# Kernel tuning notes

Measured on AMD Instinct MI355X. Metric: run time of the kernel, lower is better.

## Reference

```python
import jax, jax.numpy as jnp
import numpy as np

N = 4096
CIN = 128
COUT = 128
J = 2
SLOPE = 0.2        # LeakyReLU negative slope (GAT-style)
NEG = -9.0e15      # mask fill value from the source
ATT = J * COUT     # att_slice


def _leaky(v):
    return jnp.where(v >= 0, v, SLOPE * v)


def setup_inputs() -> dict:
    key = jax.random.key(0)
    ks = jax.random.split(key, 12)
    x = jax.random.normal(ks[0], (N, CIN), dtype=jnp.float32)

    def sparse_op(k):
        kv, km = jax.random.split(k)
        vals = jax.random.normal(kv, (N, N), dtype=jnp.float32)
        mask = jax.random.uniform(km, (N, N)) < 0.05
        return jnp.where(mask, vals, 0.0)

    Lu = sparse_op(ks[1])
    Ld = sparse_op(ks[2])
    P = jax.random.normal(ks[3], (N, N), dtype=jnp.float32) * 0.01  # harmonic projector

    s = 1.0 / np.sqrt(CIN)
    Wi_w = jax.random.uniform(ks[4], (J, CIN, COUT), minval=-s, maxval=s)
    Wi_b = jax.random.uniform(ks[5], (J, COUT), minval=-s, maxval=s)
    Ws_w = jax.random.uniform(ks[6], (J, CIN, COUT), minval=-s, maxval=s)
    Ws_b = jax.random.uniform(ks[7], (J, COUT), minval=-s, maxval=s)
    Wh_w = jax.random.uniform(ks[8], (CIN, COUT), minval=-s, maxval=s)
    Wh_b = jax.random.uniform(ks[9], (COUT,), minval=-s, maxval=s)
    att_irr = jax.random.normal(ks[10], (2 * ATT, 1), dtype=jnp.float32) * 0.1
    att_sol = jax.random.normal(ks[11], (2 * ATT, 1), dtype=jnp.float32) * 0.1
    return {"x": x, "Lu": Lu, "Ld": Ld, "P": P,
            "Wi_w": Wi_w, "Wi_b": Wi_b, "Ws_w": Ws_w, "Ws_b": Ws_b,
            "Wh_w": Wh_w, "Wh_b": Wh_b, "att_irr": att_irr, "att_sol": att_sol}


def reference(x, Lu, Ld, P, Wi_w, Wi_b, Ws_w, Ws_b, Wh_w, Wh_b, att_irr, att_sol):
    n = x.shape[0]
    # concat_j W_irr[j](x) -> [N, J*COUT] (j-major matches torch.cat along dim=1)
    x_irr = (jnp.einsum('nc,jco->njo', x, Wi_w) + Wi_b[None]).reshape(n, ATT)
    x_sol = (jnp.einsum('nc,jco->njo', x, Ws_w) + Ws_b[None]).reshape(n, ATT)

    # GAT-style scores: E[i,j] = leaky(s1[i] + s2[j])
    E_irr = _leaky(x_irr @ att_irr[:ATT] + (x_irr @ att_irr[ATT:]).T)
    E_sol = _leaky(x_sol @ att_sol[:ATT] + (x_sol @ att_sol[ATT:]).T)
    E_irr = jnp.where(Ld != 0, E_irr, NEG)
    E_sol = jnp.where(Lu != 0, E_sol, NEG)
    alpha_irr = jax.nn.softmax(E_irr, axis=1)  # dropout: eval mode -> identity
    alpha_sol = jax.nn.softmax(E_sol, axis=1)

    z = (alpha_irr @ x) @ Wi_w[0] + Wi_b[0] + (alpha_sol @ x) @ Ws_w[0] + Ws_b[0]
    for p in range(1, J):  # Laplacian-power aggregation
        alpha_irr = alpha_irr @ Ld
        alpha_sol = alpha_sol @ Lu
        z = z + (alpha_irr @ x) @ Wi_w[p] + Wi_b[p]
        z = z + (alpha_sol @ x) @ Ws_w[p] + Ws_b[p]
    z = z + (P @ x) @ Wh_w + Wh_b
    return z
```

## Files before the change

kernel.cpp:

```cpp
#include <hip/hip_runtime.h>

#define NN 4096
#define CAP 384
#define SLOPE 0.2f

#define V_OFF     0
#define C_OFF     512
#define BT_OFF    516
#define S_OFF     1024
#define HXI_OFF   32768
#define HXS_OFF   (HXI_OFF + NN*128)
#define UI_OFF    (HXS_OFF + NN*128)
#define US_OFF    (UI_OFF + NN*128)
#define XWH_OFF   (US_OFF + NN*128)
#define OI_OFF    (XWH_OFF + NN*128)
#define OS_OFF    (OI_OFF + NN*128)
#define ZP_OFF    (OS_OFF + NN*128)
#define WS_FLOATS (ZP_OFF + 8*NN*128)
#define IDX_BYTE_OFF ((size_t)WS_FLOATS * 4)
#define VAL_BYTE_OFF (IDX_BYTE_OFF + (size_t)2*NN*CAP*2)
#define CNT_BYTE_OFF (VAL_BYTE_OFF + (size_t)2*NN*CAP*4)

__global__ __launch_bounds__(128) void k_prep(
    const float* __restrict__ Wi_w, const float* __restrict__ Wi_b,
    const float* __restrict__ Ws_w, const float* __restrict__ Ws_b,
    const float* __restrict__ Wh_b, const float* __restrict__ att_irr,
    const float* __restrict__ att_sol, float* __restrict__ ws) {
  const int t = threadIdx.x;
  float v1i = 0.f, v2i = 0.f, v1s = 0.f, v2s = 0.f;
  for (int j = 0; j < 2; ++j) {
    for (int o = 0; o < 128; ++o) {
      const float wi = Wi_w[j*16384 + t*128 + o];
      const float wv = Ws_w[j*16384 + t*128 + o];
      v1i += wi * att_irr[j*128 + o];
      v2i += wi * att_irr[256 + j*128 + o];
      v1s += wv * att_sol[j*128 + o];
      v2s += wv * att_sol[256 + j*128 + o];
    }
  }
  ws[V_OFF + t]       = v1i;
  ws[V_OFF + 128 + t] = v2i;
  ws[V_OFF + 256 + t] = v1s;
  ws[V_OFF + 384 + t] = v2s;
  ws[BT_OFF + t] = Wi_b[t] + Wi_b[128 + t] + Ws_b[t] + Ws_b[128 + t] + Wh_b[t];
  if (t < 4) {
    const float* bb = (t < 2) ? Wi_b : Ws_b;
    const float* aa = ((t < 2) ? att_irr : att_sol) + ((t & 1) ? 256 : 0);
    float c = 0.f;
    for (int k = 0; k < 256; ++k) c += bb[k] * aa[k];
    ws[C_OFF + t] = c;
  }
}

__global__ __launch_bounds__(256) void k_scores(const float* __restrict__ x,
                                                float* __restrict__ ws) {
  const int wave = threadIdx.x >> 6, lane = threadIdx.x & 63;
  const int row = blockIdx.x * 4 + wave;
  const float* v = ws + V_OFF;
  const float x0 = x[row*128 + lane];
  const float x1 = x[row*128 + 64 + lane];
  float p0 = x0 * v[lane]       + x1 * v[64 + lane];
  float p1 = x0 * v[128 + lane] + x1 * v[192 + lane];
  float p2 = x0 * v[256 + lane] + x1 * v[320 + lane];
  float p3 = x0 * v[384 + lane] + x1 * v[448 + lane];
  #pragma unroll
  for (int off = 32; off; off >>= 1) {
    p0 += __shfl_down(p0, off);
    p1 += __shfl_down(p1, off);
    p2 += __shfl_down(p2, off);
    p3 += __shfl_down(p3, off);
  }
  if (lane == 0) {
    ws[S_OFF + row]          = p0 + ws[C_OFF + 0];
    ws[S_OFF + NN + row]     = p1 + ws[C_OFF + 1];
    ws[S_OFF + 2*NN + row]   = p2 + ws[C_OFF + 2];
    ws[S_OFF + 3*NN + row]   = p3 + ws[C_OFF + 3];
  }
}

__global__ __launch_bounds__(256) void k_zero(int* __restrict__ cnt) {
  cnt[blockIdx.x * 256 + threadIdx.x] = 0;
}

__global__ __launch_bounds__(256) void k_csr(
    const float* __restrict__ Ld, const float* __restrict__ Lu,
    int* __restrict__ cntbuf, unsigned short* __restrict__ idxb,
    float* __restrict__ valb) {
  const int w = threadIdx.x >> 6, lane = threadIdx.x & 63;
  const int W = blockIdx.x * 4 + w;
  const int br = W >> 14;
  const int row = (W >> 2) & (NN - 1);
  const int quarter = W & 3;
  const float4* __restrict__ L4 =
      (const float4*)((br ? Lu : Ld) + (size_t)row * NN + quarter * 1024);
  float4 lv[4];
  #pragma unroll
  for (int i = 0; i < 4; ++i) lv[i] = L4[i*64 + lane];

  unsigned long long m[16];
  int runs[16];
  int run = 0;
  #pragma unroll
  for (int i = 0; i < 4; ++i)
    #pragma unroll
    for (int c = 0; c < 4; ++c) {
      const int r = i*4 + c;
      m[r] = __ballot((&lv[i].x)[c] != 0.f);
      runs[r] = run;
      run += (int)__popcll(m[r]);
    }
  int base = 0;
  if (lane == 0 && run) base = atomicAdd(&cntbuf[br*NN + row], run);
  base = __shfl(base, 0);
  const size_t rb = (size_t)(br*NN + row) * CAP;
  const unsigned long long lmask = (1ull << lane) - 1ull;
  #pragma unroll
  for (int i = 0; i < 4; ++i)
    #pragma unroll
    for (int c = 0; c < 4; ++c) {
      const int r = i*4 + c;
      const float v = (&lv[i].x)[c];
      if (v != 0.f) {
        const int pos = base + runs[r] + (int)__popcll(m[r] & lmask);
        if (pos < CAP) {
          idxb[rb + pos] = (unsigned short)(quarter*1024 + (i*64 + lane)*4 + c);
          valb[rb + pos] = v;
        }
      }
    }
}

__global__ __launch_bounds__(256) void k_gather_hx(
    const float* __restrict__ Ld, const float* __restrict__ Lu,
    const float* __restrict__ x, float* __restrict__ ws,
    const unsigned short* __restrict__ idxb, const float* __restrict__ valb,
    const int* __restrict__ cntbuf) {
  const int w = threadIdx.x >> 6, lane = threadIdx.x & 63;
  const int W = blockIdx.x * 4 + w;
  const int br = W >> 12;
  const int row = W & (NN - 1);
  const float2* __restrict__ x2 = (const float2*)x;
  float2* __restrict__ Hx2 = (float2*)(ws + (br ? HXS_OFF : HXI_OFF));
  const int cnt = cntbuf[br*NN + row];
  float a0 = 0.f, a1 = 0.f;
  if (cnt <= CAP) {
    const size_t rb = (size_t)(br*NN + row) * CAP;
    int jv[6]; float vv[6];
    #pragma unroll
    for (int s = 0; s < 6; ++s) {
      const int p = s*64 + lane;
      const bool in = p < cnt;
      jv[s] = in ? (int)idxb[rb + p] : 0;
      vv[s] = in ? valb[rb + p] : 0.f;
    }
    #pragma unroll
    for (int s = 0; s < 6; ++s) {
      if (s*64 < cnt) {
        const int qn = min(64, cnt - s*64);
        const int jvs = jv[s]; const float vvs = vv[s];
        int q = 0;
        for (; q + 8 <= qn; q += 8) {
          const int j0=__shfl(jvs,q+0), j1=__shfl(jvs,q+1), j2=__shfl(jvs,q+2), j3=__shfl(jvs,q+3);
          const int j4=__shfl(jvs,q+4), j5=__shfl(jvs,q+5), j6=__shfl(jvs,q+6), j7=__shfl(jvs,q+7);
          const float v0=__shfl(vvs,q+0), v1=__shfl(vvs,q+1), v2=__shfl(vvs,q+2), v3=__shfl(vvs,q+3);
          const float v4=__shfl(vvs,q+4), v5=__shfl(vvs,q+5), v6=__shfl(vvs,q+6), v7=__shfl(vvs,q+7);
          const float2 g0=x2[j0*64+lane], g1=x2[j1*64+lane], g2=x2[j2*64+lane], g3=x2[j3*64+lane];
          const float2 g4=x2[j4*64+lane], g5=x2[j5*64+lane], g6=x2[j6*64+lane], g7=x2[j7*64+lane];
          a0+=v0*g0.x; a1+=v0*g0.y; a0+=v1*g1.x; a1+=v1*g1.y;
          a0+=v2*g2.x; a1+=v2*g2.y; a0+=v3*g3.x; a1+=v3*g3.y;
          a0+=v4*g4.x; a1+=v4*g4.y; a0+=v5*g5.x; a1+=v5*g5.y;
          a0+=v6*g6.x; a1+=v6*g6.y; a0+=v7*g7.x; a1+=v7*g7.y;
        }
        for (; q < qn; ++q) {
          const int j = __shfl(jvs, q); const float v = __shfl(vvs, q);
          const float2 g = x2[j*64+lane];
          a0 += v*g.x; a1 += v*g.y;
        }
      }
    }
  } else {
    const float* __restrict__ Lrow = (br ? Lu : Ld) + (size_t)row * NN;
    for (int j = 0; j < NN; ++j) {
      const float v = Lrow[j];
      if (v != 0.f) { const float2 g = x2[j*64+lane]; a0 += v*g.x; a1 += v*g.y; }
    }
  }
  float2 o; o.x = a0; o.y = a1;
  Hx2[row*64 + lane] = o;
}

__global__ __launch_bounds__(256) void k_ugemm(
    const float* __restrict__ x, const float* __restrict__ Wi_w,
    const float* __restrict__ Ws_w, const float* __restrict__ Wh_w,
    float* __restrict__ ws) {
  const int rb = blockIdx.x;
  const int sel = blockIdx.y;
  const float* A[2]; const float* W[2]; int npass; float* out;
  if (sel == 0)      { A[0]=x; W[0]=Wi_w; A[1]=ws+HXI_OFF; W[1]=Wi_w+16384; npass=2; out=ws+UI_OFF; }
  else if (sel == 1) { A[0]=x; W[0]=Ws_w; A[1]=ws+HXS_OFF; W[1]=Ws_w+16384; npass=2; out=ws+US_OFF; }
  else               { A[0]=x; W[0]=Wh_w; A[1]=nullptr;    W[1]=nullptr;    npass=1; out=ws+XWH_OFF; }

  __shared__ __align__(16) float At[32][33];
  __shared__ __align__(16) float Wt[32][132];
  const int t = threadIdx.x;
  const int rg = t >> 4, cg = t & 15;
  const int r0 = rb * 32;
  float acc[2][8];
  #pragma unroll
  for (int i = 0; i < 2; ++i)
    #pragma unroll
    for (int j = 0; j < 8; ++j) acc[i][j] = 0.f;

  for (int ps = 0; ps < npass; ++ps) {
    const float* __restrict__ Ap = A[ps];
    const float* __restrict__ Wp = W[ps];
    for (int k0 = 0; k0 < 128; k0 += 32) {
      __syncthreads();
      { const int row = t >> 3, kq = t & 7;
        const float4 av = *(const float4*)&Ap[(r0 + row)*128 + k0 + kq*4];
        At[row][kq*4+0] = av.x; At[row][kq*4+1] = av.y;
        At[row][kq*4+2] = av.z; At[row][kq*4+3] = av.w; }
      #pragma unroll
      for (int l = 0; l < 4; ++l) {
        const int idx = t + l*256;
        const int kr = idx >> 5, c4 = idx & 31;
        const float4 wv = *(const float4*)&Wp[(k0 + kr)*128 + c4*4];
        Wt[kr][c4*4+0] = wv.x; Wt[kr][c4*4+1] = wv.y;
        Wt[kr][c4*4+2] = wv.z; Wt[kr][c4*4+3] = wv.w;
      }
      __syncthreads();
      #pragma unroll
      for (int k = 0; k < 32; ++k) {
        const float a0 = At[rg*2 + 0][k];
        const float a1 = At[rg*2 + 1][k];
        const float4 b0 = *(const float4*)&Wt[k][cg*8];
        const float4 b1 = *(const float4*)&Wt[k][cg*8 + 4];
        acc[0][0] += a0*b0.x; acc[0][1] += a0*b0.y; acc[0][2] += a0*b0.z; acc[0][3] += a0*b0.w;
        acc[0][4] += a0*b1.x; acc[0][5] += a0*b1.y; acc[0][6] += a0*b1.z; acc[0][7] += a0*b1.w;
        acc[1][0] += a1*b0.x; acc[1][1] += a1*b0.y; acc[1][2] += a1*b0.z; acc[1][3] += a1*b0.w;
        acc[1][4] += a1*b1.x; acc[1][5] += a1*b1.y; acc[1][6] += a1*b1.z; acc[1][7] += a1*b1.w;
      }
    }
  }
  #pragma unroll
  for (int i = 0; i < 2; ++i) {
    const int r = r0 + rg*2 + i;
    #pragma unroll
    for (int j = 0; j < 8; ++j) out[r*128 + cg*8 + j] = acc[i][j];
  }
}

__global__ __launch_bounds__(256) void k_pgemm(const float* __restrict__ P,
                                               const float* __restrict__ ws,
                                               float* __restrict__ zpart) {
  const int rbl = blockIdx.x;
  const int kz  = blockIdx.y;
  const float* __restrict__ Xw = ws + XWH_OFF;

  __shared__ __align__(16) float At[32][68];
  __shared__ __align__(16) float Xt[32][132];
  const int t = threadIdx.x;
  const int rg = t >> 4, cg = t & 15;
  const int r0 = rbl * 64;
  const int kbase = kz * 512;
  float acc[4][8];
  #pragma unroll
  for (int i = 0; i < 4; ++i)
    #pragma unroll
    for (int j = 0; j < 8; ++j) acc[i][j] = 0.f;

  for (int k0 = kbase; k0 < kbase + 512; k0 += 32) {
    __syncthreads();
    #pragma unroll
    for (int l = 0; l < 2; ++l) {
      const int idx = t + l*256;
      const int row = idx >> 3, kq = idx & 7;
      const float4 pv = *(const float4*)&P[(size_t)(r0 + row)*NN + k0 + kq*4];
      At[kq*4+0][row] = pv.x; At[kq*4+1][row] = pv.y;
      At[kq*4+2][row] = pv.z; At[kq*4+3][row] = pv.w;
    }
    #pragma unroll
    for (int l = 0; l < 4; ++l) {
      const int idx = t + l*256;
      const int kr = idx >> 5, c4 = idx & 31;
      const float4 xv = *(const float4*)&Xw[(k0 + kr)*128 + c4*4];
      Xt[kr][c4*4+0] = xv.x; Xt[kr][c4*4+1] = xv.y;
      Xt[kr][c4*4+2] = xv.z; Xt[kr][c4*4+3] = xv.w;
    }
    __syncthreads();
    #pragma unroll
    for (int k = 0; k < 32; ++k) {
      const float4 a  = *(const float4*)&At[k][rg*4];
      const float4 b0 = *(const float4*)&Xt[k][cg*8];
      const float4 b1 = *(const float4*)&Xt[k][cg*8 + 4];
      acc[0][0] += a.x*b0.x; acc[0][1] += a.x*b0.y; acc[0][2] += a.x*b0.z; acc[0][3] += a.x*b0.w;
      acc[0][4] += a.x*b1.x; acc[0][5] += a.x*b1.y; acc[0][6] += a.x*b1.z; acc[0][7] += a.x*b1.w;
      acc[1][0] += a.y*b0.x; acc[1][1] += a.y*b0.y; acc[1][2] += a.y*b0.z; acc[1][3] += a.y*b0.w;
      acc[1][4] += a.y*b1.x; acc[1][5] += a.y*b1.y; acc[1][6] += a.y*b1.z; acc[1][7] += a.y*b1.w;
      acc[2][0] += a.z*b0.x; acc[2][1] += a.z*b0.y; acc[2][2] += a.z*b0.z; acc[2][3] += a.z*b0.w;
      acc[2][4] += a.z*b1.x; acc[2][5] += a.z*b1.y; acc[2][6] += a.z*b1.z; acc[2][7] += a.z*b1.w;
      acc[3][0] += a.w*b0.x; acc[3][1] += a.w*b0.y; acc[3][2] += a.w*b0.z; acc[3][3] += a.w*b0.w;
      acc[3][4] += a.w*b1.x; acc[3][5] += a.w*b1.y; acc[3][6] += a.w*b1.z; acc[3][7] += a.w*b1.w;
    }
  }
  float* __restrict__ zp = zpart + (size_t)kz * NN * 128;
  #pragma unroll
  for (int i = 0; i < 4; ++i) {
    const int r = r0 + rg*4 + i;
    #pragma unroll
    for (int j = 0; j < 8; ++j) zp[r*128 + cg*8 + j] = acc[i][j];
  }
}

__global__ __launch_bounds__(256) void k_attn(
    const float* __restrict__ Ld, const float* __restrict__ Lu,
    float* __restrict__ ws, const unsigned short* __restrict__ idxb,
    const int* __restrict__ cntbuf) {
  const int w = threadIdx.x >> 6, lane = threadIdx.x & 63;
  const int W = blockIdx.x * 4 + w;
  const int br = W >> 12;
  const int row = W & (NN - 1);
  const float2* __restrict__ U2 = (const float2*)(ws + (br ? US_OFF : UI_OFF));
  float2* __restrict__ O2 = (float2*)(ws + (br ? OS_OFF : OI_OFF));
  const float s1 = ws[S_OFF + (br ? 2*NN : 0) + row];
  const float* __restrict__ s2a = ws + S_OFF + (br ? 3*NN : NN);
  const int cnt = cntbuf[br*NN + row];
  float a0 = 0.f, a1 = 0.f;
  float den = 0.f;

  if (cnt > 0 && cnt <= CAP) {
    const size_t rb = (size_t)(br*NN + row) * CAP;
    int jv[6]; float ev[6];
    float dl = 0.f;
    #pragma unroll
    for (int s = 0; s < 6; ++s) {
      const int p = s*64 + lane;
      if (p < cnt) {
        const int j = (int)idxb[rb + p];
        const float sc = s1 + s2a[j];
        const float e = expf(sc >= 0.f ? sc : SLOPE * sc);
        jv[s] = j; ev[s] = e; dl += e;
      } else { jv[s] = 0; ev[s] = 0.f; }
    }
    #pragma unroll
    for (int off = 32; off; off >>= 1) dl += __shfl_xor(dl, off);
    den = dl;
    #pragma unroll
    for (int s = 0; s < 6; ++s) {
      if (s*64 < cnt) {
        const int qn = min(64, cnt - s*64);
        const int jvs = jv[s]; const float evs = ev[s];
        int q = 0;
        for (; q + 8 <= qn; q += 8) {
          const int j0=__shfl(jvs,q+0), j1=__shfl(jvs,q+1), j2=__shfl(jvs,q+2), j3=__shfl(jvs,q+3);
          const int j4=__shfl(jvs,q+4), j5=__shfl(jvs,q+5), j6=__shfl(jvs,q+6), j7=__shfl(jvs,q+7);
          const float e0=__shfl(evs,q+0), e1=__shfl(evs,q+1), e2=__shfl(evs,q+2), e3=__shfl(evs,q+3);
          const float e4=__shfl(evs,q+4), e5=__shfl(evs,q+5), e6=__shfl(evs,q+6), e7=__shfl(evs,q+7);
          const float2 g0=U2[j0*64+lane], g1=U2[j1*64+lane], g2=U2[j2*64+lane], g3=U2[j3*64+lane];
          const float2 g4=U2[j4*64+lane], g5=U2[j5*64+lane], g6=U2[j6*64+lane], g7=U2[j7*64+lane];
          a0+=e0*g0.x; a1+=e0*g0.y; a0+=e1*g1.x; a1+=e1*g1.y;
          a0+=e2*g2.x; a1+=e2*g2.y; a0+=e3*g3.x; a1+=e3*g3.y;
          a0+=e4*g4.x; a1+=e4*g4.y; a0+=e5*g5.x; a1+=e5*g5.y;
          a0+=e6*g6.x; a1+=e6*g6.y; a0+=e7*g7.x; a1+=e7*g7.y;
        }
        for (; q < qn; ++q) {
          const int j = __shfl(jvs, q); const float e = __shfl(evs, q);
          const float2 g = U2[j*64+lane];
          a0 += e*g.x; a1 += e*g.y;
        }
      }
    }
    float2 o; o.x = a0 / den; o.y = a1 / den;
    O2[row*64 + lane] = o;
  } else if (cnt == 0) {
    for (int j = 0; j < NN; ++j) { const float2 g = U2[j*64+lane]; a0 += g.x; a1 += g.y; }
    float2 o; o.x = a0 * (1.f/NN); o.y = a1 * (1.f/NN);
    O2[row*64 + lane] = o;
  } else {
    const float* __restrict__ Lrow = (br ? Lu : Ld) + (size_t)row * NN;
    for (int j = 0; j < NN; ++j) {
      const float v = Lrow[j];
      if (v != 0.f) {
        const float sc = s1 + s2a[j];
        const float e = expf(sc >= 0.f ? sc : SLOPE * sc);
        const float2 g = U2[j*64+lane];
        a0 += e*g.x; a1 += e*g.y; den += e;
      }
    }
    float2 o; o.x = a0 / den; o.y = a1 / den;
    O2[row*64 + lane] = o;
  }
}

__global__ __launch_bounds__(256) void k_combine(const float* __restrict__ ws,
                                                 float* __restrict__ z) {
  const int i = blockIdx.x * 256 + threadIdx.x;
  const int col = i & 127;
  float acc = ws[BT_OFF + col] + ws[OI_OFF + i] + ws[OS_OFF + i];
  #pragma unroll
  for (int kz = 0; kz < 8; ++kz) acc += ws[ZP_OFF + kz*NN*128 + i];
  z[i] = acc;
}

extern "C" void kernel_launch(void* const* d_in, const int* in_sizes, int n_in,
                              void* d_out, int out_size, void* d_ws, size_t ws_size,
                              hipStream_t stream) {
  const float* x       = (const float*)d_in[0];
  const float* Lu      = (const float*)d_in[1];
  const float* Ld      = (const float*)d_in[2];
  const float* P       = (const float*)d_in[3];
  const float* Wi_w    = (const float*)d_in[4];
  const float* Wi_b    = (const float*)d_in[5];
  const float* Ws_w    = (const float*)d_in[6];
  const float* Ws_b    = (const float*)d_in[7];
  const float* Wh_w    = (const float*)d_in[8];
  const float* Wh_b    = (const float*)d_in[9];
  const float* att_irr = (const float*)d_in[10];
  const float* att_sol = (const float*)d_in[11];
  float* z  = (float*)d_out;
  float* ws = (float*)d_ws;
  unsigned short* idxb = (unsigned short*)((char*)d_ws + IDX_BYTE_OFF);
  float*          valb = (float*)((char*)d_ws + VAL_BYTE_OFF);
  int*            cntb = (int*)((char*)d_ws + CNT_BYTE_OFF);

  k_prep<<<1, 128, 0, stream>>>(Wi_w, Wi_b, Ws_w, Ws_b, Wh_b, att_irr, att_sol, ws);
  k_scores<<<1024, 256, 0, stream>>>(x, ws);
  k_zero<<<32, 256, 0, stream>>>(cntb);
  k_csr<<<8192, 256, 0, stream>>>(Ld, Lu, cntb, idxb, valb);
  k_gather_hx<<<2048, 256, 0, stream>>>(Ld, Lu, x, ws, idxb, valb, cntb);
  {
    dim3 g(128, 3);
    k_ugemm<<<g, 256, 0, stream>>>(x, Wi_w, Ws_w, Wh_w, ws);
  }
  {
    dim3 g(64, 8);
    k_pgemm<<<g, 256, 0, stream>>>(P, ws, ws + ZP_OFF);
  }
  k_attn<<<2048, 256, 0, stream>>>(Ld, Lu, ws, idxb, cntb);
  k_combine<<<NN * 128 / 256, 256, 0, stream>>>(ws, z);
}
```

Before: 415.7 us.

## Use bf16 MFMA for dense P @ XWh projection with transposed bf16 operand

Replaces the scalar FP32 shared-memory tiled GEMM for P @ (x Wh) with MFMA 16x16x32 bf16 instructions. A new kernel first transposes XWh into a bf16 [128 x N] layout so each lane can load 8 contiguous K values. P rows are loaded straight from global memory, converted to bf16 in registers, and prefetched one step ahead. This moves the large dense GEMM onto the matrix cores and drops the LDS staging. In exchange it adds a transpose kernel and bf16 rounding error on P and XWh.

```diff
diff --git a/kernel.cpp b/kernel.cpp
--- a/kernel.cpp
+++ b/kernel.cpp
@@ -3,6 +3,15 @@
 #define NN 4096
 #define CAP 384
 #define SLOPE 0.2f
+
+typedef __attribute__((ext_vector_type(8))) short bf16x8;
+typedef __attribute__((ext_vector_type(4))) float f32x4;
+
+static __device__ __forceinline__ short f2bf(float f) {
+  unsigned u = __builtin_bit_cast(unsigned, f);
+  unsigned r = (u + 0x7fffu + ((u >> 16) & 1u)) >> 16;
+  return (short)r;
+}
 
 #define V_OFF     0
 #define C_OFF     512
@@ -20,6 +29,7 @@
 #define IDX_BYTE_OFF ((size_t)WS_FLOATS * 4)
 #define VAL_BYTE_OFF (IDX_BYTE_OFF + (size_t)2*NN*CAP*2)
 #define CNT_BYTE_OFF (VAL_BYTE_OFF + (size_t)2*NN*CAP*4)
+#define XWT_BYTE_OFF (CNT_BYTE_OFF + (size_t)2*NN*4)
 
 __global__ __launch_bounds__(128) void k_prep(
     const float* __restrict__ Wi_w, const float* __restrict__ Wi_b,
@@ -250,66 +260,77 @@
   }
 }
 
+__global__ __launch_bounds__(256) void k_xwt(const float* __restrict__ ws,
+                                             unsigned short* __restrict__ XwT) {
+  const float* __restrict__ Xw = ws + XWH_OFF;
+  __shared__ float tile[64][133];
+  const int t = threadIdx.x;
+  const int k0 = blockIdx.x * 64;
+  #pragma unroll
+  for (int lp = 0; lp < 8; ++lp) {
+    const int idx = t + lp*256;
+    const int r = idx >> 5, c4 = idx & 31;
+    const float4 v = *(const float4*)&Xw[(size_t)(k0 + r)*128 + c4*4];
+    tile[r][c4*4+0]=v.x; tile[r][c4*4+1]=v.y; tile[r][c4*4+2]=v.z; tile[r][c4*4+3]=v.w;
+  }
+  __syncthreads();
+  const int n = t >> 1, seg = t & 1;
+  unsigned out[16];
+  #pragma unroll
+  for (int q = 0; q < 16; ++q) {
+    const int kk = seg*32 + q*2;
+    const unsigned lo = (unsigned)(unsigned short)f2bf(tile[kk][n]);
+    const unsigned hi = (unsigned)(unsigned short)f2bf(tile[kk+1][n]);
+    out[q] = lo | (hi << 16);
+  }
+  unsigned* __restrict__ dst = (unsigned*)&XwT[(size_t)n*NN + k0 + seg*32];
+  #pragma unroll
+  for (int q = 0; q < 16; ++q) dst[q] = out[q];
+}
+
 __global__ __launch_bounds__(256) void k_pgemm(const float* __restrict__ P,
-                                               const float* __restrict__ ws,
+                                               const unsigned short* __restrict__ XwT,
                                                float* __restrict__ zpart) {
-  const int rbl = blockIdx.x;
-  const int kz  = blockIdx.y;
-  const float* __restrict__ Xw = ws + XWH_OFF;
-
-  __shared__ __align__(16) float At[32][68];
-  __shared__ __align__(16) float Xt[32][132];
   const int t = threadIdx.x;
-  const int rg = t >> 4, cg = t & 15;
-  const int r0 = rbl * 64;
+  const int w = t >> 6, l = t & 63;
+  const int quad = l >> 4, m16 = l & 15;
+  const int r0 = blockIdx.x * 64;
+  const int kz = blockIdx.y;
+  const int row = r0 + w*16 + m16;
+  const float* __restrict__ Arow = P + (size_t)row * NN;
   const int kbase = kz * 512;
-  float acc[4][8];
-  #pragma unroll
-  for (int i = 0; i < 4; ++i)
-    #pragma unroll
-    for (int j = 0; j < 8; ++j) acc[i][j] = 0.f;
-
-  for (int k0 = kbase; k0 < kbase + 512; k0 += 32) {
-    __syncthreads();
-    #pragma unroll
-    for (int l = 0; l < 2; ++l) {
-      const int idx = t + l*256;
-      const int row = idx >> 3, kq = idx & 7;
-      const float4 pv = *(const float4*)&P[(size_t)(r0 + row)*NN + k0 + kq*4];
-      At[kq*4+0][row] = pv.x; At[kq*4+1][row] = pv.y;
-      At[kq*4+2][row] = pv.z; At[kq*4+3][row] = pv.w;
-    }
-    #pragma unroll
-    for (int l = 0; l < 4; ++l) {
-      const int idx = t + l*256;
-      const int kr = idx >> 5, c4 = idx & 31;
-      const float4 xv = *(const float4*)&Xw[(k0 + kr)*128 + c4*4];
-      Xt[kr][c4*4+0] = xv.x; Xt[kr][c4*4+1] = xv.y;
-      Xt[kr][c4*4+2] = xv.z; Xt[kr][c4*4+3] = xv.w;
-    }
-    __syncthreads();
-    #pragma unroll
-    for (int k = 0; k < 32; ++k) {
-      const float4 a  = *(const float4*)&At[k][rg*4];
-      const float4 b0 = *(const float4*)&Xt[k][cg*8];
-      const float4 b1 = *(const float4*)&Xt[k][cg*8 + 4];
-      acc[0][0] += a.x*b0.x; acc[0][1] += a.x*b0.y; acc[0][2] += a.x*b0.z; acc[0][3] += a.x*b0.w;
-      acc[0][4] += a.x*b1.x; acc[0][5] += a.x*b1.y; acc[0][6] += a.x*b1.z; acc[0][7] += a.x*b1.w;
-      acc[1][0] += a.y*b0.x; acc[1][1] += a.y*b0.y; acc[1][2] += a.y*b0.z; acc[1][3] += a.y*b0.w;
-      acc[1][4] += a.y*b1.x; acc[1][5] += a.y*b1.y; acc[1][6] += a.y*b1.z; acc[1][7] += a.y*b1.w;
-      acc[2][0] += a.z*b0.x; acc[2][1] += a.z*b0.y; acc[2][2] += a.z*b0.z; acc[2][3] += a.z*b0.w;
-      acc[2][4] += a.z*b1.x; acc[2][5] += a.z*b1.y; acc[2][6] += a.z*b1.z; acc[2][7] += a.z*b1.w;
-      acc[3][0] += a.w*b0.x; acc[3][1] += a.w*b0.y; acc[3][2] += a.w*b0.z; acc[3][3] += a.w*b0.w;
-      acc[3][4] += a.w*b1.x; acc[3][5] += a.w*b1.y; acc[3][6] += a.w*b1.z; acc[3][7] += a.w*b1.w;
-    }
+
+  f32x4 acc[8];
+  #pragma unroll
+  for (int nt = 0; nt < 8; ++nt) acc[nt] = (f32x4){0.f, 0.f, 0.f, 0.f};
+
+  float4 a0 = *(const float4*)&Arow[kbase + quad*8];
+  float4 a1 = *(const float4*)&Arow[kbase + quad*8 + 4];
+  for (int ks = 0; ks < 16; ++ks) {
+    const int k0 = kbase + ks*32;
+    bf16x8 bf[8];
+    #pragma unroll
+    for (int nt = 0; nt < 8; ++nt)
+      bf[nt] = *(const bf16x8*)&XwT[(size_t)(nt*16 + m16) * NN + k0 + quad*8];
+    float4 na0, na1;
+    if (ks < 15) {
+      na0 = *(const float4*)&Arow[k0 + 32 + quad*8];
+      na1 = *(const float4*)&Arow[k0 + 32 + quad*8 + 4];
+    }
+    bf16x8 af;
+    af[0]=f2bf(a0.x); af[1]=f2bf(a0.y); af[2]=f2bf(a0.z); af[3]=f2bf(a0.w);
+    af[4]=f2bf(a1.x); af[5]=f2bf(a1.y); af[6]=f2bf(a1.z); af[7]=f2bf(a1.w);
+    #pragma unroll
+    for (int nt = 0; nt < 8; ++nt)
+      acc[nt] = __builtin_amdgcn_mfma_f32_16x16x32_bf16(af, bf[nt], acc[nt], 0, 0, 0);
+    a0 = na0; a1 = na1;
   }
   float* __restrict__ zp = zpart + (size_t)kz * NN * 128;
   #pragma unroll
-  for (int i = 0; i < 4; ++i) {
-    const int r = r0 + rg*4 + i;
-    #pragma unroll
-    for (int j = 0; j < 8; ++j) zp[r*128 + cg*8 + j] = acc[i][j];
-  }
+  for (int nt = 0; nt < 8; ++nt)
+    #pragma unroll
+    for (int r = 0; r < 4; ++r)
+      zp[(size_t)(r0 + w*16 + quad*4 + r)*128 + nt*16 + m16] = acc[nt][r];
 }
 
 __global__ __launch_bounds__(256) void k_attn(
@@ -422,6 +443,7 @@
   unsigned short* idxb = (unsigned short*)((char*)d_ws + IDX_BYTE_OFF);
   float*          valb = (float*)((char*)d_ws + VAL_BYTE_OFF);
   int*            cntb = (int*)((char*)d_ws + CNT_BYTE_OFF);
+  unsigned short* xwtb = (unsigned short*)((char*)d_ws + XWT_BYTE_OFF);
 
   k_prep<<<1, 128, 0, stream>>>(Wi_w, Wi_b, Ws_w, Ws_b, Wh_b, att_irr, att_sol, ws);
   k_scores<<<1024, 256, 0, stream>>>(x, ws);
@@ -432,9 +454,10 @@
     dim3 g(128, 3);
     k_ugemm<<<g, 256, 0, stream>>>(x, Wi_w, Ws_w, Wh_w, ws);
   }
+  k_xwt<<<64, 256, 0, stream>>>(ws, xwtb);
   {
     dim3 g(64, 8);
-    k_pgemm<<<g, 256, 0, stream>>>(P, ws, ws + ZP_OFF);
+    k_pgemm<<<g, 256, 0, stream>>>(P, xwtb, ws + ZP_OFF);
   }
   k_attn<<<2048, 256, 0, stream>>>(Ld, Lu, ws, idxb, cntb);
   k_combine<<<NN * 128 / 256, 256, 0, stream>>>(ws, z);
```

Measured after the change: 410.8 us. About the same (-1.2%).
